# Kernel optimization log

Measured on AMD Instinct MI355X. Metric: run time of the kernel, lower is better.

The kernel has to match this reference:

```python
import jax, jax.numpy as jnp
import numpy as np

H = 16
D_MODEL = 1024
D_HID = 50  # hidden width of the 1->50->1 mask MLP


def setup_inputs() -> dict:
    key = jax.random.key(0)
    ks = jax.random.split(key, 16)
    B, S, D = 16, 768, D_MODEL
    n, nk = 512, 256  # code length n, redundancy n-k; S = n + nk
    inp = {
        "query": jax.random.normal(ks[0], (B, S, D), jnp.float32),
        "key": jax.random.normal(ks[1], (B, S, D), jnp.float32),
        "value": jax.random.normal(ks[2], (B, S, D), jnp.float32),
        "pc_matrix": jax.random.uniform(ks[3], (nk, n), jnp.float32),
        # four Linear(d_model, d_model) layers: q, k, v, out. Stored so that y = x @ W + b.
        "Wq": jax.random.normal(ks[4], (D, D), jnp.float32) * 0.02,
        "bq": jnp.zeros((D,), jnp.float32),
        "Wk": jax.random.normal(ks[5], (D, D), jnp.float32) * 0.02,
        "bk": jnp.zeros((D,), jnp.float32),
        "Wv": jax.random.normal(ks[6], (D, D), jnp.float32) * 0.02,
        "bv": jnp.zeros((D,), jnp.float32),
        "Wo": jax.random.normal(ks[7], (D, D), jnp.float32) * 0.02,
        "bo": jnp.zeros((D,), jnp.float32),
        # one_d_mapping: Linear(1,50) -> ReLU -> Linear(50,1)
        "mw1": jax.random.normal(ks[8], (1, D_HID), jnp.float32) * 0.5,
        "mb1": jax.random.normal(ks[9], (D_HID,), jnp.float32) * 0.1,
        "mw2": jax.random.normal(ks[10], (D_HID, 1), jnp.float32) * 0.5,
        "mb2": jnp.zeros((1,), jnp.float32),
    }
    return inp


def _mask_from_pc(pc, mw1, mb1, mw2, mb2):
    # pc: (nk, n). Build (S, S) block matrix, S = n + nk.
    nknk = pc @ pc.T            # (nk, nk)
    nn = pc.T @ pc              # (n, n)
    top = jnp.concatenate([nn, pc.T], axis=1)     # (n, S)
    bot = jnp.concatenate([pc, nknk], axis=1)     # (nk, S)
    M = jnp.concatenate([top, bot], axis=0)       # (S, S)
    # elementwise 1->50->1 MLP
    h = jax.nn.relu(M[..., None] * mw1[0] + mb1)  # (S, S, 50)
    out = h @ mw2 + mb2                           # (S, S, 1)
    return out[..., 0]                            # (S, S)


def reference(query, key, value, pc_matrix, Wq, bq, Wk, bk, Wv, bv, Wo, bo,
              mw1, mb1, mw2, mb2):
    B, S, D = query.shape
    dk = D // H
    q = (query @ Wq + bq).reshape(B, S, H, dk).transpose(0, 2, 1, 3)
    k = (key @ Wk + bk).reshape(B, S, H, dk).transpose(0, 2, 1, 3)
    v = (value @ Wv + bv).reshape(B, S, H, dk).transpose(0, 2, 1, 3)
    scores = jnp.einsum("bhqd,bhkd->bhqk", q, k) / jnp.sqrt(jnp.float32(dk))
    mask = _mask_from_pc(pc_matrix, mw1, mb1, mw2, mb2)  # (S, S)
    scores = scores * mask[None, None]  # multiplicative float mask
    p = jax.nn.softmax(scores, axis=-1)  # dropout is identity in eval mode
    x = jnp.einsum("bhqk,bhkd->bhqd", p, v)
    x = x.transpose(0, 2, 1, 3).reshape(B, S, D)
    return x @ Wo + bo
```

## Files before the change

kernel.cpp:

```cpp
#include <hip/hip_runtime.h>
#include <stdint.h>

typedef _Float16 f16;
typedef _Float16 f16x8 __attribute__((ext_vector_type(8)));
typedef float f32x4 __attribute__((ext_vector_type(4)));

union U4 { uint4 u; f16 h[8]; };

#define GLOAD16(g, l)                                                         \
  __builtin_amdgcn_global_load_lds(                                           \
      (const __attribute__((address_space(1))) void*)(g),                     \
      (__attribute__((address_space(3))) void*)(l), 16, 0, 0)

__global__ __launch_bounds__(256) void k_wt(const float* __restrict__ W0,
                                            const float* __restrict__ W1,
                                            const float* __restrict__ W2,
                                            const float* __restrict__ W3,
                                            f16* __restrict__ T0, f16* __restrict__ T1,
                                            f16* __restrict__ T2, f16* __restrict__ T3) {
    __shared__ f16 tile[64 * 65];
    int z = blockIdx.z;
    const float* W = z == 0 ? W0 : z == 1 ? W1 : z == 2 ? W2 : W3;
    f16* Wt = z == 0 ? T0 : z == 1 ? T1 : z == 2 ? T2 : T3;
    int t = threadIdx.x;
    int k0 = blockIdx.x * 64, n0 = blockIdx.y * 64;
    #pragma unroll
    for (int i = 0; i < 4; i++) {
        int cid = t + i * 256;
        int row = cid >> 4, c4 = cid & 15;
        float4 v = *(const float4*)(W + (size_t)(k0 + row) * 1024 + n0 + c4 * 4);
        tile[(c4 * 4 + 0) * 65 + row] = (f16)v.x;
        tile[(c4 * 4 + 1) * 65 + row] = (f16)v.y;
        tile[(c4 * 4 + 2) * 65 + row] = (f16)v.z;
        tile[(c4 * 4 + 3) * 65 + row] = (f16)v.w;
    }
    __syncthreads();
    #pragma unroll
    for (int i = 0; i < 2; i++) {
        int cid = t + i * 256;
        int nr = cid >> 3, kc = cid & 7;
        U4 u;
        #pragma unroll
        for (int j = 0; j < 8; j++) u.h[j] = tile[nr * 65 + kc * 8 + j];
        *(uint4*)(Wt + (size_t)(n0 + nr) * 1024 + k0 + kc * 8) = u.u;
    }
}

__global__ __launch_bounds__(256) void k_cvt(const float* __restrict__ in,
                                             f16* __restrict__ out) {
    size_t id = (size_t)blockIdx.x * 256 + threadIdx.x;
    float4 a = *(const float4*)(in + id * 8);
    float4 b = *(const float4*)(in + id * 8 + 4);
    U4 u;
    u.h[0] = (f16)a.x; u.h[1] = (f16)a.y; u.h[2] = (f16)a.z; u.h[3] = (f16)a.w;
    u.h[4] = (f16)b.x; u.h[5] = (f16)b.y; u.h[6] = (f16)b.z; u.h[7] = (f16)b.w;
    *(uint4*)(out + id * 8) = u.u;
}

template <int TRANS>
__global__ __launch_bounds__(256) void k_gram(const float* __restrict__ pc,
                                              float* __restrict__ out) {
    constexpr int N = TRANS ? 256 : 512;
    constexpr int K = TRANS ? 512 : 256;
    __shared__ float As[16][68];
    __shared__ float Bs[16][68];
    int t = threadIdx.x;
    int i0 = blockIdx.x * 64, j0 = blockIdx.y * 64;
    int ty = t >> 4, tx = t & 15;
    float acc[4][4];
    #pragma unroll
    for (int r = 0; r < 4; r++)
        #pragma unroll
        for (int c = 0; c < 4; c++) acc[r][c] = 0.f;

    for (int kt = 0; kt < K; kt += 16) {
        if (TRANS == 0) {
            int k = t >> 4, c4 = t & 15;
            float4 va = *(const float4*)(pc + (size_t)(kt + k) * 512 + i0 + c4 * 4);
            float4 vb = *(const float4*)(pc + (size_t)(kt + k) * 512 + j0 + c4 * 4);
            *(float4*)&As[k][c4 * 4] = va;
            *(float4*)&Bs[k][c4 * 4] = vb;
        } else {
            int r = t >> 2, kc = t & 3;
            float4 va = *(const float4*)(pc + (size_t)(i0 + r) * 512 + kt + kc * 4);
            As[kc * 4 + 0][r] = va.x; As[kc * 4 + 1][r] = va.y;
            As[kc * 4 + 2][r] = va.z; As[kc * 4 + 3][r] = va.w;
            float4 vb = *(const float4*)(pc + (size_t)(j0 + r) * 512 + kt + kc * 4);
            Bs[kc * 4 + 0][r] = vb.x; Bs[kc * 4 + 1][r] = vb.y;
            Bs[kc * 4 + 2][r] = vb.z; Bs[kc * 4 + 3][r] = vb.w;
        }
        __syncthreads();
        #pragma unroll
        for (int u = 0; u < 16; u++) {
            float4 av = *(const float4*)&As[u][ty * 4];
            float4 bv = *(const float4*)&Bs[u][tx * 4];
            float aa[4] = {av.x, av.y, av.z, av.w};
            float bb[4] = {bv.x, bv.y, bv.z, bv.w};
            #pragma unroll
            for (int r = 0; r < 4; r++)
                #pragma unroll
                for (int c = 0; c < 4; c++) acc[r][c] += aa[r] * bb[c];
        }
        __syncthreads();
    }
    #pragma unroll
    for (int r = 0; r < 4; r++)
        #pragma unroll
        for (int c = 0; c < 4; c++)
            out[(size_t)(i0 + ty * 4 + r) * N + j0 + tx * 4 + c] = acc[r][c];
}

__global__ __launch_bounds__(256) void k_mask(const float* __restrict__ pc,
                                              const float* __restrict__ nn,
                                              const float* __restrict__ nknk,
                                              const float* __restrict__ mw1,
                                              const float* __restrict__ mb1,
                                              const float* __restrict__ mw2,
                                              const float* __restrict__ mb2,
                                              float* __restrict__ maskp) {
    __shared__ float w1[50], b1[50], w2[50];
    int t = threadIdx.x;
    if (t < 50) { w1[t] = mw1[t]; b1[t] = mb1[t]; w2[t] = mw2[t]; }
    __syncthreads();
    int id = blockIdx.x * 256 + t;
    int i = id / 768, j = id - i * 768;
    float M;
    if (i < 512) M = (j < 512) ? nn[(size_t)i * 512 + j] : pc[(size_t)(j - 512) * 512 + i];
    else         M = (j < 512) ? pc[(size_t)(i - 512) * 512 + j]
                               : nknk[(size_t)(i - 512) * 256 + (j - 512)];
    float acc = mb2[0];
    #pragma unroll 10
    for (int u = 0; u < 50; u++) acc += fmaxf(M * w1[u] + b1[u], 0.f) * w2[u];
    maskp[id] = acc;
}

__global__ __launch_bounds__(256) void k_vt(const f16* __restrict__ Vh,
                                            f16* __restrict__ VT) {
    __shared__ f16 tile[64][72];
    int t = threadIdx.x;
    int s0 = blockIdx.x * 64;
    int bh = blockIdx.y, b = bh >> 4, h = bh & 15;
    #pragma unroll
    for (int p = 0; p < 2; p++) {
        int cid = t + p * 256;
        int s = cid >> 3, dc = cid & 7;
        *(uint4*)&tile[s][dc * 8] =
            *(const uint4*)(Vh + ((size_t)b * 768 + s0 + s) * 1024 + h * 64 + dc * 8);
    }
    __syncthreads();
    #pragma unroll
    for (int p = 0; p < 2; p++) {
        int cid = t + p * 256;
        int d = cid >> 3, sc = cid & 7;
        U4 u;
        #pragma unroll
        for (int j = 0; j < 8; j++) u.h[j] = tile[sc * 8 + j][d];
        *(uint4*)(VT + ((size_t)bh * 64 + d) * 768 + s0 + sc * 8) = u.u;
    }
}

template <int MODE>
__global__ __launch_bounds__(256) void k_gemm(const f16* __restrict__ A,
                                              const f16* __restrict__ Bt,
                                              const float* __restrict__ bias,
                                              void* out0v, void* out1v) {
    __shared__ f16 As[128 * 32];
    __shared__ f16 Bs[128 * 32];
    int t = threadIdx.x;
    int w = t >> 6, lane = t & 63, l15 = lane & 15, quad = lane >> 4;
    int wm = w >> 1, wn = w & 1;
    int row0 = blockIdx.x * 128, n0 = blockIdx.y * 128;

    int m0 = w * 16 + (lane >> 2);
    int m1 = m0 + 64;
    int ks0 = (lane & 3) ^ ((m0 >> 1) & 3);
    int ks1 = (lane & 3) ^ ((m1 >> 1) & 3);
    const f16* gA0 = A + (size_t)(row0 + m0) * 1024 + ks0 * 8;
    const f16* gA1 = A + (size_t)(row0 + m1) * 1024 + ks1 * 8;
    const f16* gB0 = Bt + (size_t)(n0 + m0) * 1024 + ks0 * 8;
    const f16* gB1 = Bt + (size_t)(n0 + m1) * 1024 + ks1 * 8;
    f16* lA = As + w * 512;
    f16* lB = Bs + w * 512;
    int sw = (l15 >> 1) & 3;

    f32x4 acc[4][4];
    #pragma unroll
    for (int mi = 0; mi < 4; mi++)
        #pragma unroll
        for (int ni = 0; ni < 4; ni++) acc[mi][ni] = (f32x4){0.f, 0.f, 0.f, 0.f};

    for (int kt = 0; kt < 32; kt++) {
        int k0 = kt * 32;
        GLOAD16(gA0 + k0, lA);
        GLOAD16(gA1 + k0, lA + 2048);
        GLOAD16(gB0 + k0, lB);
        GLOAD16(gB1 + k0, lB + 2048);
        __syncthreads();
        f16x8 af[4], bf_[4];
        #pragma unroll
        for (int mi = 0; mi < 4; mi++)
            af[mi] = *(const f16x8*)((const char*)As +
                     (size_t)(wm * 64 + mi * 16 + l15) * 64 + ((quad ^ sw) << 4));
        #pragma unroll
        for (int ni = 0; ni < 4; ni++)
            bf_[ni] = *(const f16x8*)((const char*)Bs +
                      (size_t)(wn * 64 + ni * 16 + l15) * 64 + ((quad ^ sw) << 4));
        #pragma unroll
        for (int mi = 0; mi < 4; mi++)
            #pragma unroll
            for (int ni = 0; ni < 4; ni++)
                acc[mi][ni] = __builtin_amdgcn_mfma_f32_16x16x32_f16(af[mi], bf_[ni],
                                                                     acc[mi][ni], 0, 0, 0);
        __syncthreads();
    }
    #pragma unroll
    for (int mi = 0; mi < 4; mi++) {
        #pragma unroll
        for (int ni = 0; ni < 4; ni++) {
            int col = n0 + wn * 64 + ni * 16 + l15;
            float bv = bias[col];
            #pragma unroll
            for (int r = 0; r < 4; r++) {
                int row = row0 + wm * 64 + mi * 16 + quad * 4 + r;
                float v = acc[mi][ni][r] + bv;
                size_t idx = (size_t)row * 1024 + col;
                if (MODE == 0) {
                    ((f16*)out0v)[idx] = (f16)v;
                } else if (MODE == 1) {
                    f16 hi = (f16)v;
                    ((f16*)out0v)[idx] = hi;
                    ((f16*)out1v)[idx] = (f16)(v - (float)hi);
                } else {
                    ((float*)out0v)[idx] = v;
                }
            }
        }
    }
}

__global__ __launch_bounds__(256) void k_attn(const f16* __restrict__ Qhi,
                                              const f16* __restrict__ Qlo,
                                              const f16* __restrict__ Khi,
                                              const f16* __restrict__ Klo,
                                              const f16* __restrict__ VT,
                                              const float* __restrict__ maskp,
                                              f16* __restrict__ Xout) {
    __shared__ f16 Ksh[32 * 64];
    __shared__ f16 Ksl[32 * 64];
    __shared__ f16 Vt[64 * 32];
    __shared__ f16 Ps[4][16 * 40];
    int t = threadIdx.x;
    int w = t >> 6, lane = t & 63, l15 = lane & 15, quad = lane >> 4;
    int q0 = blockIdx.x * 64;
    int bh = blockIdx.y; int b = bh >> 4, h = bh & 15;
    const size_t base = ((size_t)b * 768) * 1024 + h * 64;

    int krow = w * 8 + (lane >> 3);
    int kslot = (lane & 7) ^ (krow & 7);
    const f16* gKh = Khi + base + (size_t)krow * 1024 + kslot * 8;
    const f16* gKl = Klo + base + (size_t)krow * 1024 + kslot * 8;
    f16* lKh = Ksh + w * 512;
    f16* lKl = Ksl + w * 512;
    int vd = w * 16 + (lane >> 2);
    int vslot = (lane & 3) ^ ((vd >> 1) & 3);
    const f16* gV = VT + ((size_t)bh * 64 + vd) * 768 + vslot * 8;
    f16* lV = Vt + w * 512;

    int swv = (l15 >> 1) & 3;
    int kx = l15 & 7;

    f16x8 qh[2], ql[2];
    int qrow = q0 + w * 16 + l15;
    #pragma unroll
    for (int c = 0; c < 2; c++) {
        qh[c] = *(const f16x8*)(Qhi + base + (size_t)qrow * 1024 + c * 32 + quad * 8);
        ql[c] = *(const f16x8*)(Qlo + base + (size_t)qrow * 1024 + c * 32 + quad * 8);
    }
    float mst[4], lst[4];
    f32x4 o[4];
    #pragma unroll
    for (int r = 0; r < 4; r++) { mst[r] = -1e30f; lst[r] = 0.f; }
    #pragma unroll
    for (int ni = 0; ni < 4; ni++) o[ni] = (f32x4){0.f, 0.f, 0.f, 0.f};

    for (int kt = 0; kt < 24; kt++) {
        int k0 = kt * 32;
        __syncthreads();
        GLOAD16(gKh + (size_t)k0 * 1024, lKh);
        GLOAD16(gKl + (size_t)k0 * 1024, lKl);
        GLOAD16(gV + k0, lV);
        __syncthreads();

        float sv[2][4];
        #pragma unroll
        for (int kn = 0; kn < 2; kn++) {
            f32x4 s = (f32x4){0.f, 0.f, 0.f, 0.f};
            int key = kn * 16 + l15;
            #pragma unroll
            for (int c = 0; c < 2; c++) {
                int slot = ((c << 2) + quad) ^ kx;
                f16x8 kh = *(const f16x8*)((const char*)Ksh + (size_t)key * 128 + (slot << 4));
                f16x8 kl = *(const f16x8*)((const char*)Ksl + (size_t)key * 128 + (slot << 4));
                s = __builtin_amdgcn_mfma_f32_16x16x32_f16(qh[c], kh, s, 0, 0, 0);
                s = __builtin_amdgcn_mfma_f32_16x16x32_f16(ql[c], kh, s, 0, 0, 0);
                s = __builtin_amdgcn_mfma_f32_16x16x32_f16(qh[c], kl, s, 0, 0, 0);
            }
            #pragma unroll
            for (int r = 0; r < 4; r++) {
                float mv = maskp[(q0 + w * 16 + quad * 4 + r) * 768 + k0 + kn * 16 + l15];
                sv[kn][r] = s[r] * 0.125f * mv;
            }
        }
        #pragma unroll
        for (int r = 0; r < 4; r++) {
            float tm = fmaxf(sv[0][r], sv[1][r]);
            tm = fmaxf(tm, __shfl_xor(tm, 1));
            tm = fmaxf(tm, __shfl_xor(tm, 2));
            tm = fmaxf(tm, __shfl_xor(tm, 4));
            tm = fmaxf(tm, __shfl_xor(tm, 8));
            float mn = fmaxf(mst[r], tm);
            float alpha = __expf(mst[r] - mn);
            mst[r] = mn;
            float p0 = __expf(sv[0][r] - mn), p1 = __expf(sv[1][r] - mn);
            float rs = p0 + p1;
            rs += __shfl_xor(rs, 1);
            rs += __shfl_xor(rs, 2);
            rs += __shfl_xor(rs, 4);
            rs += __shfl_xor(rs, 8);
            lst[r] = lst[r] * alpha + rs;
            #pragma unroll
            for (int ni = 0; ni < 4; ni++) o[ni][r] *= alpha;
            Ps[w][(quad * 4 + r) * 40 + l15] = (f16)p0;
            Ps[w][(quad * 4 + r) * 40 + 16 + l15] = (f16)p1;
        }
        asm volatile("s_waitcnt lgkmcnt(0)" ::: "memory");
        f16x8 pa = *(const f16x8*)&Ps[w][l15 * 40 + quad * 8];
        #pragma unroll
        for (int ni = 0; ni < 4; ni++) {
            f16x8 vb = *(const f16x8*)((const char*)Vt +
                       (size_t)(ni * 16 + l15) * 64 + ((quad ^ swv) << 4));
            o[ni] = __builtin_amdgcn_mfma_f32_16x16x32_f16(pa, vb, o[ni], 0, 0, 0);
        }
    }
    #pragma unroll
    for (int ni = 0; ni < 4; ni++)
        #pragma unroll
        for (int r = 0; r < 4; r++) {
            int row = q0 + w * 16 + quad * 4 + r;
            int col = ni * 16 + l15;
            Xout[((size_t)b * 768 + row) * 1024 + h * 64 + col] = (f16)(o[ni][r] / lst[r]);
        }
}

extern "C" void kernel_launch(void* const* d_in, const int* in_sizes, int n_in,
                              void* d_out, int out_size, void* d_ws, size_t ws_size,
                              hipStream_t stream) {
    (void)in_sizes; (void)n_in; (void)out_size; (void)ws_size;
    const float* query = (const float*)d_in[0];
    const float* key   = (const float*)d_in[1];
    const float* value = (const float*)d_in[2];
    const float* pc    = (const float*)d_in[3];
    const float* Wq    = (const float*)d_in[4];
    const float* bq    = (const float*)d_in[5];
    const float* Wk    = (const float*)d_in[6];
    const float* bk    = (const float*)d_in[7];
    const float* Wv    = (const float*)d_in[8];
    const float* bv    = (const float*)d_in[9];
    const float* Wo    = (const float*)d_in[10];
    const float* bo    = (const float*)d_in[11];
    const float* mw1   = (const float*)d_in[12];
    const float* mb1   = (const float*)d_in[13];
    const float* mw2   = (const float*)d_in[14];
    const float* mb2   = (const float*)d_in[15];

    char* p = (char*)d_ws;
    auto take = [&](size_t bytes) -> char* {
        char* r = p; p += (bytes + 255) & ~(size_t)255; return r;
    };
    const size_t NTOK = 12288, DM = 1024;
    float* maskb = (float*)take(768 * 768 * 4);
    float* nnb   = (float*)take(512 * 512 * 4);
    float* nknkb = (float*)take(256 * 256 * 4);
    f16* Wqt = (f16*)take(DM * DM * 2);
    f16* Wkt = (f16*)take(DM * DM * 2);
    f16* Wvt = (f16*)take(DM * DM * 2);
    f16* Wot = (f16*)take(DM * DM * 2);
    f16* buf1 = (f16*)take(NTOK * DM * 2);
    f16* Qhi = (f16*)take(NTOK * DM * 2);
    f16* Qlo = (f16*)take(NTOK * DM * 2);
    f16* Khi = (f16*)take(NTOK * DM * 2);
    f16* Klo = (f16*)take(NTOK * DM * 2);
    f16* Vhb = (f16*)take(NTOK * DM * 2);
    f16* VTb = (f16*)take(NTOK * DM * 2);

    k_wt<<<dim3(16, 16, 4), 256, 0, stream>>>(Wq, Wk, Wv, Wo, Wqt, Wkt, Wvt, Wot);
    k_gram<0><<<dim3(8, 8), 256, 0, stream>>>(pc, nnb);
    k_gram<1><<<dim3(4, 4), 256, 0, stream>>>(pc, nknkb);
    k_mask<<<2304, 256, 0, stream>>>(pc, nnb, nknkb, mw1, mb1, mw2, mb2, maskb);

    dim3 gg(96, 8);
    k_cvt<<<6144, 256, 0, stream>>>(query, buf1);
    k_gemm<1><<<gg, 256, 0, stream>>>(buf1, Wqt, bq, Qhi, Qlo);
    k_cvt<<<6144, 256, 0, stream>>>(key, buf1);
    k_gemm<1><<<gg, 256, 0, stream>>>(buf1, Wkt, bk, Khi, Klo);
    k_cvt<<<6144, 256, 0, stream>>>(value, buf1);
    k_gemm<0><<<gg, 256, 0, stream>>>(buf1, Wvt, bv, Vhb, nullptr);

    k_vt<<<dim3(12, 256), 256, 0, stream>>>(Vhb, VTb);

    dim3 ag(12, 256);
    k_attn<<<ag, 256, 0, stream>>>(Qhi, Qlo, Khi, Klo, VTb, maskb, buf1);

    k_gemm<2><<<gg, 256, 0, stream>>>(buf1, Wot, bo, d_out, nullptr);
}
```

Baseline: 640.7 us.

## Double-buffer attention K/V tiles, widen key tile, lazy rescale, XCD-aware block remap

The attention kernel now processes 64-key tiles with double-buffered LDS staging, so the next tile's K/V loads are issued while the current tile is computed, and the mask values are prefetched into registers. Online softmax rescaling is skipped unless a row's max grows by more than 8, which removes most alpha multiplies at the cost of larger intermediate exponent ranges. GEMM and attention grids become 1D with an index remap that groups related blocks per XCD (id&7) to improve L2 reuse. LDS use grows substantially, which may reduce occupancy.

```diff
diff --git a/kernel.cpp b/kernel.cpp
--- a/kernel.cpp
+++ b/kernel.cpp
@@ -169,7 +169,10 @@
     int t = threadIdx.x;
     int w = t >> 6, lane = t & 63, l15 = lane & 15, quad = lane >> 4;
     int wm = w >> 1, wn = w & 1;
-    int row0 = blockIdx.x * 128, n0 = blockIdx.y * 128;
+    int id = blockIdx.x;
+    int rest = id >> 3;
+    int row0 = ((id & 7) * 12 + rest % 12) * 128;
+    int n0 = (rest / 12) * 128;
 
     int m0 = w * 16 + (lane >> 2);
     int m1 = m0 + 64;
@@ -245,29 +248,20 @@
                                               const f16* __restrict__ VT,
                                               const float* __restrict__ maskp,
                                               f16* __restrict__ Xout) {
-    __shared__ f16 Ksh[32 * 64];
-    __shared__ f16 Ksl[32 * 64];
-    __shared__ f16 Vt[64 * 32];
-    __shared__ f16 Ps[4][16 * 40];
+    __shared__ f16 Ksh[2][64 * 64];
+    __shared__ f16 Ksl[2][64 * 64];
+    __shared__ f16 Vs[2][64 * 64];
+    __shared__ f16 Ps[4][16 * 64];
     int t = threadIdx.x;
     int w = t >> 6, lane = t & 63, l15 = lane & 15, quad = lane >> 4;
-    int q0 = blockIdx.x * 64;
-    int bh = blockIdx.y; int b = bh >> 4, h = bh & 15;
+    int id = blockIdx.x;
+    int bh = (id & 7) + ((id >> 3) / 12) * 8;
+    int q0 = ((id >> 3) % 12) * 64;
+    int b = bh >> 4, h = bh & 15;
     const size_t base = ((size_t)b * 768) * 1024 + h * 64;
 
-    int krow = w * 8 + (lane >> 3);
-    int kslot = (lane & 7) ^ (krow & 7);
-    const f16* gKh = Khi + base + (size_t)krow * 1024 + kslot * 8;
-    const f16* gKl = Klo + base + (size_t)krow * 1024 + kslot * 8;
-    f16* lKh = Ksh + w * 512;
-    f16* lKl = Ksl + w * 512;
-    int vd = w * 16 + (lane >> 2);
-    int vslot = (lane & 3) ^ ((vd >> 1) & 3);
-    const f16* gV = VT + ((size_t)bh * 64 + vd) * 768 + vslot * 8;
-    f16* lV = Vt + w * 512;
-
-    int swv = (l15 >> 1) & 3;
-    int kx = l15 & 7;
+    int srow = lane >> 3;
+    int sslot = lane & 7;
 
     f16x8 qh[2], ql[2];
     int qrow = q0 + w * 16 + l15;
@@ -283,64 +277,113 @@
     #pragma unroll
     for (int ni = 0; ni < 4; ni++) o[ni] = (f32x4){0.f, 0.f, 0.f, 0.f};
 
-    for (int kt = 0; kt < 24; kt++) {
-        int k0 = kt * 32;
-        __syncthreads();
-        GLOAD16(gKh + (size_t)k0 * 1024, lKh);
-        GLOAD16(gKl + (size_t)k0 * 1024, lKl);
-        GLOAD16(gV + k0, lV);
-        __syncthreads();
-
-        float sv[2][4];
-        #pragma unroll
-        for (int kn = 0; kn < 2; kn++) {
+    auto STAGE = [&](int bsel, int k0) {
+        #pragma unroll
+        for (int p = 0; p < 2; p++) {
+            int row = w * 16 + p * 8 + srow;
+            int ss = sslot ^ (row & 7);
+            GLOAD16(Khi + base + (size_t)(k0 + row) * 1024 + ss * 8,
+                    &Ksh[bsel][w * 1024 + p * 512]);
+            GLOAD16(Klo + base + (size_t)(k0 + row) * 1024 + ss * 8,
+                    &Ksl[bsel][w * 1024 + p * 512]);
+            GLOAD16(VT + ((size_t)bh * 64 + row) * 768 + k0 + ss * 8,
+                    &Vs[bsel][w * 1024 + p * 512]);
+        }
+    };
+
+    STAGE(0, 0);
+    __syncthreads();
+    int buf = 0;
+    int kx = l15 & 7;
+
+    for (int kt = 0; kt < 12; kt++) {
+        int k0 = kt * 64;
+        float mv[4][4];
+        #pragma unroll
+        for (int kn = 0; kn < 4; kn++)
+            #pragma unroll
+            for (int r = 0; r < 4; r++)
+                mv[kn][r] = maskp[(q0 + w * 16 + quad * 4 + r) * 768 + k0 + kn * 16 + l15];
+        if (kt < 11) STAGE(buf ^ 1, k0 + 64);
+
+        float sv[4][4];
+        #pragma unroll
+        for (int kn = 0; kn < 4; kn++) {
             f32x4 s = (f32x4){0.f, 0.f, 0.f, 0.f};
             int key = kn * 16 + l15;
             #pragma unroll
             for (int c = 0; c < 2; c++) {
                 int slot = ((c << 2) + quad) ^ kx;
-                f16x8 kh = *(const f16x8*)((const char*)Ksh + (size_t)key * 128 + (slot << 4));
-                f16x8 kl = *(const f16x8*)((const char*)Ksl + (size_t)key * 128 + (slot << 4));
+                f16x8 kh = *(const f16x8*)((const char*)&Ksh[buf][0] +
+                                           (size_t)key * 128 + (slot << 4));
+                f16x8 kl = *(const f16x8*)((const char*)&Ksl[buf][0] +
+                                           (size_t)key * 128 + (slot << 4));
                 s = __builtin_amdgcn_mfma_f32_16x16x32_f16(qh[c], kh, s, 0, 0, 0);
                 s = __builtin_amdgcn_mfma_f32_16x16x32_f16(ql[c], kh, s, 0, 0, 0);
                 s = __builtin_amdgcn_mfma_f32_16x16x32_f16(qh[c], kl, s, 0, 0, 0);
             }
             #pragma unroll
-            for (int r = 0; r < 4; r++) {
-                float mv = maskp[(q0 + w * 16 + quad * 4 + r) * 768 + k0 + kn * 16 + l15];
-                sv[kn][r] = s[r] * 0.125f * mv;
-            }
-        }
+            for (int r = 0; r < 4; r++) sv[kn][r] = s[r] * 0.125f * mv[kn][r];
+        }
+
+        float tmr[4];
+        bool need = false;
         #pragma unroll
         for (int r = 0; r < 4; r++) {
-            float tm = fmaxf(sv[0][r], sv[1][r]);
+            float tm = fmaxf(fmaxf(sv[0][r], sv[1][r]), fmaxf(sv[2][r], sv[3][r]));
             tm = fmaxf(tm, __shfl_xor(tm, 1));
             tm = fmaxf(tm, __shfl_xor(tm, 2));
             tm = fmaxf(tm, __shfl_xor(tm, 4));
             tm = fmaxf(tm, __shfl_xor(tm, 8));
-            float mn = fmaxf(mst[r], tm);
-            float alpha = __expf(mst[r] - mn);
-            mst[r] = mn;
-            float p0 = __expf(sv[0][r] - mn), p1 = __expf(sv[1][r] - mn);
-            float rs = p0 + p1;
+            tmr[r] = tm;
+            need = need || (tm > mst[r] + 8.f);
+        }
+        if (__any(need)) {
+            #pragma unroll
+            for (int r = 0; r < 4; r++) {
+                float mn = fmaxf(mst[r], tmr[r]);
+                float alpha = __expf(mst[r] - mn);
+                mst[r] = mn;
+                lst[r] *= alpha;
+                #pragma unroll
+                for (int ni = 0; ni < 4; ni++) o[ni][r] *= alpha;
+            }
+        }
+        #pragma unroll
+        for (int r = 0; r < 4; r++) {
+            int row = quad * 4 + r;
+            float p0 = __expf(sv[0][r] - mst[r]);
+            float p1 = __expf(sv[1][r] - mst[r]);
+            float p2 = __expf(sv[2][r] - mst[r]);
+            float p3 = __expf(sv[3][r] - mst[r]);
+            float rs = (p0 + p1) + (p2 + p3);
             rs += __shfl_xor(rs, 1);
             rs += __shfl_xor(rs, 2);
             rs += __shfl_xor(rs, 4);
             rs += __shfl_xor(rs, 8);
-            lst[r] = lst[r] * alpha + rs;
-            #pragma unroll
-            for (int ni = 0; ni < 4; ni++) o[ni][r] *= alpha;
-            Ps[w][(quad * 4 + r) * 40 + l15] = (f16)p0;
-            Ps[w][(quad * 4 + r) * 40 + 16 + l15] = (f16)p1;
+            lst[r] += rs;
+            int rl = l15 >> 3, re = l15 & 7, rx = row & 7;
+            Ps[w][row * 64 + ((0 + rl) ^ rx) * 8 + re] = (f16)p0;
+            Ps[w][row * 64 + ((2 + rl) ^ rx) * 8 + re] = (f16)p1;
+            Ps[w][row * 64 + ((4 + rl) ^ rx) * 8 + re] = (f16)p2;
+            Ps[w][row * 64 + ((6 + rl) ^ rx) * 8 + re] = (f16)p3;
         }
         asm volatile("s_waitcnt lgkmcnt(0)" ::: "memory");
-        f16x8 pa = *(const f16x8*)&Ps[w][l15 * 40 + quad * 8];
-        #pragma unroll
-        for (int ni = 0; ni < 4; ni++) {
-            f16x8 vb = *(const f16x8*)((const char*)Vt +
-                       (size_t)(ni * 16 + l15) * 64 + ((quad ^ swv) << 4));
-            o[ni] = __builtin_amdgcn_mfma_f32_16x16x32_f16(pa, vb, o[ni], 0, 0, 0);
-        }
+        #pragma unroll
+        for (int c = 0; c < 2; c++) {
+            int pslot = ((c << 2) + quad) ^ kx;
+            f16x8 pa = *(const f16x8*)((const char*)&Ps[w][0] +
+                                       (size_t)l15 * 128 + (pslot << 4));
+            #pragma unroll
+            for (int ni = 0; ni < 4; ni++) {
+                int d = ni * 16 + l15;
+                f16x8 vb = *(const f16x8*)((const char*)&Vs[buf][0] +
+                                           (size_t)d * 128 + (pslot << 4));
+                o[ni] = __builtin_amdgcn_mfma_f32_16x16x32_f16(pa, vb, o[ni], 0, 0, 0);
+            }
+        }
+        __syncthreads();
+        buf ^= 1;
     }
     #pragma unroll
     for (int ni = 0; ni < 4; ni++)
@@ -398,18 +441,16 @@
     k_gram<1><<<dim3(4, 4), 256, 0, stream>>>(pc, nknkb);
     k_mask<<<2304, 256, 0, stream>>>(pc, nnb, nknkb, mw1, mb1, mw2, mb2, maskb);
 
-    dim3 gg(96, 8);
     k_cvt<<<6144, 256, 0, stream>>>(query, buf1);
-    k_gemm<1><<<gg, 256, 0, stream>>>(buf1, Wqt, bq, Qhi, Qlo);
+    k_gemm<1><<<768, 256, 0, stream>>>(buf1, Wqt, bq, Qhi, Qlo);
     k_cvt<<<6144, 256, 0, stream>>>(key, buf1);
-    k_gemm<1><<<gg, 256, 0, stream>>>(buf1, Wkt, bk, Khi, Klo);
+    k_gemm<1><<<768, 256, 0, stream>>>(buf1, Wkt, bk, Khi, Klo);
     k_cvt<<<6144, 256, 0, stream>>>(value, buf1);
-    k_gemm<0><<<gg, 256, 0, stream>>>(buf1, Wvt, bv, Vhb, nullptr);
+    k_gemm<0><<<768, 256, 0, stream>>>(buf1, Wvt, bv, Vhb, nullptr);
 
     k_vt<<<dim3(12, 256), 256, 0, stream>>>(Vhb, VTb);
 
-    dim3 ag(12, 256);
-    k_attn<<<ag, 256, 0, stream>>>(Qhi, Qlo, Khi, Klo, VTb, maskb, buf1);
-
-    k_gemm<2><<<gg, 256, 0, stream>>>(buf1, Wot, bo, d_out, nullptr);
-}
+    k_attn<<<3072, 256, 0, stream>>>(Qhi, Qlo, Khi, Klo, VTb, maskb, buf1);
+
+    k_gemm<2><<<768, 256, 0, stream>>>(buf1, Wot, bo, d_out, nullptr);
+}
```

New measurement: 631.0 us. No clear change (-1.5%).
